# Performance work log

Measured on AMD Instinct MI355X. Metric: run time of the kernel, lower is better.

## Reference

```python
import jax, jax.numpy as jnp
import numpy as np

HARD_RATIO = 0.5
HARD_WEIGHT = 0.5
B, Q, D = 1024, 32, 512


def _l2norm(x):
    return x / jnp.linalg.norm(x, axis=-1, keepdims=True)


def setup_inputs() -> dict:
    key = jax.random.key(0)
    k1, k2 = jax.random.split(key)
    fusion_feats = _l2norm(jax.random.normal(k1, (B, D), dtype=jnp.float32))
    target_feats = _l2norm(jax.random.normal(k2, (B, Q, D), dtype=jnp.float32))
    temp = jnp.float32(0.07)
    return {"fusion_feats": fusion_feats, "target_feats": target_feats, "temp": temp}


def reference(fusion_feats, target_feats, temp):
    b = fusion_feats.shape[0]
    # sim[i, j, q] = fusion[i] . target[j, q]  -> max over query tokens q
    sim = jnp.einsum('id,jqd->ijq', fusion_feats, target_feats)  # (B, B, Q)
    sim_max = jnp.max(sim, axis=-1) / temp                        # (B, B)

    # standard InfoNCE with diagonal labels
    loss_standard = -jnp.mean(jnp.diagonal(jax.nn.log_softmax(sim_max, axis=-1)))

    # online hard-negative mining: per-row top-k over off-diagonal entries
    num_hard = max(1, int(b * HARD_RATIO))
    diag_mask = jnp.eye(b, dtype=bool)
    masked = jnp.where(diag_mask, -jnp.inf, sim_max)
    hard_sims, _ = jax.lax.top_k(masked, num_hard)                # (B, num_hard)
    pos = jnp.diagonal(sim_max)                                    # (B,)
    # -log(exp(pos) / (exp(pos) + sum exp(hard))) = logsumexp([pos, hard]) - pos
    lse = jax.nn.logsumexp(jnp.concatenate([pos[:, None], hard_sims], axis=1), axis=1)
    hard_loss_online = jnp.mean(lse - pos)

    total_loss = loss_standard + HARD_WEIGHT * hard_loss_online
    return total_loss
```

## Files before the change

### kernel.cpp

```cpp
#include <hip/hip_runtime.h>
#include <hip/hip_bf16.h>
#include <math.h>

typedef unsigned short u16;
typedef unsigned char u8;
typedef unsigned int u32;
typedef __attribute__((ext_vector_type(4))) float f32x4;
typedef __attribute__((ext_vector_type(8))) int i32x8;

__global__ void cvt_fused(const float* __restrict__ F, const float* __restrict__ T,
                          u32* __restrict__ Fb, u32* __restrict__ Tb,
                          float* __restrict__ out) {
    const int idx = blockIdx.x * blockDim.x + threadIdx.x;
    if (idx == 0) out[0] = 0.f;
    const float* s;
    u32* d;
    int i;
    if (idx < 65536) { s = F; d = Fb; i = idx; }
    else             { s = T; d = Tb; i = idx - 65536; }
    const float4 v0 = *(const float4*)(s + (size_t)i * 8);
    const float4 v1 = *(const float4*)(s + (size_t)i * 8 + 4);
    int lo = __builtin_amdgcn_cvt_pk_fp8_f32(v0.x * 16.f, v0.y * 16.f, 0, false);
    lo     = __builtin_amdgcn_cvt_pk_fp8_f32(v0.z * 16.f, v0.w * 16.f, lo, true);
    int hi = __builtin_amdgcn_cvt_pk_fp8_f32(v1.x * 16.f, v1.y * 16.f, 0, false);
    hi     = __builtin_amdgcn_cvt_pk_fp8_f32(v1.z * 16.f, v1.w * 16.f, hi, true);
    uint2 o; o.x = (u32)lo; o.y = (u32)hi;
    ((uint2*)d)[i] = o;
}

#define GLB_AS __attribute__((address_space(1)))
#define LDS_AS __attribute__((address_space(3)))

__device__ __forceinline__ void gload_lds16(const void* g, void* l) {
    __builtin_amdgcn_global_load_lds((const GLB_AS void*)g, (LDS_AS void*)l, 16, 0, 0);
}

__device__ __forceinline__ i32x8 mk8(int4 a, int4 b) {
    i32x8 r;
    r[0] = a.x; r[1] = a.y; r[2] = a.z; r[3] = a.w;
    r[4] = b.x; r[5] = b.y; r[6] = b.z; r[7] = b.w;
    return r;
}

__global__ __launch_bounds__(256, 2)
void gemm_max(const u8* __restrict__ A, const u8* __restrict__ B,
              const float* __restrict__ temp_ptr, float* __restrict__ sim) {
    __shared__ __align__(16) u8 lA[128 * 128];
    __shared__ __align__(16) u8 lB[128 * 128];
    const int bn = blockIdx.x;
    const int bm = blockIdx.y;
    const int tid  = threadIdx.x;
    const int wave = tid >> 6;
    const int lane = tid & 63;
    const int wm = wave >> 1;
    const int wn = wave & 1;

    f32x4 acc[4][4] = {};

    const int srow = lane >> 3;
    const int sch  = (lane & 7) ^ srow;
    const u8* gA0 = A + (size_t)(bm * 128 + wave * 8 + srow) * 512 + sch * 16;
    const u8* gB0 = B + (size_t)(bn * 128 + wave * 8 + srow) * 512 + sch * 16;
    u8* dA = lA + wave * 1024;
    u8* dB = lB + wave * 1024;

    const int frow = lane & 15;
    const int fq   = lane >> 4;

    for (int k0 = 0; k0 < 512; k0 += 128) {
#pragma unroll
        for (int j = 0; j < 4; ++j) {
            gload_lds16(gA0 + k0 + j * 16384, dA + j * 4096);
            gload_lds16(gB0 + k0 + j * 16384, dB + j * 4096);
        }
        __syncthreads();

        i32x8 bf[4];
#pragma unroll
        for (int t = 0; t < 4; ++t) {
            const int rb = wn * 64 + t * 16 + frow;
            const int bb = ((rb >> 3) << 10) + ((rb & 7) << 7);
            int4 p0 = *(const int4*)&lB[bb + ((((fq << 1))     ^ (rb & 7)) << 4)];
            int4 p1 = *(const int4*)&lB[bb + ((((fq << 1) | 1) ^ (rb & 7)) << 4)];
            bf[t] = mk8(p0, p1);
        }
#pragma unroll
        for (int mt = 0; mt < 4; ++mt) {
            const int ra = wm * 64 + mt * 16 + frow;
            const int ba = ((ra >> 3) << 10) + ((ra & 7) << 7);
            int4 q0 = *(const int4*)&lA[ba + ((((fq << 1))     ^ (ra & 7)) << 4)];
            int4 q1 = *(const int4*)&lA[ba + ((((fq << 1) | 1) ^ (ra & 7)) << 4)];
            const i32x8 af = mk8(q0, q1);
#pragma unroll
            for (int nt = 0; nt < 4; ++nt)
                acc[mt][nt] = __builtin_amdgcn_mfma_scale_f32_16x16x128_f8f6f4(
                    af, bf[nt], acc[mt][nt],
                    0, 0,
                    0, 0x7F,
                    0, 0x7F);
        }
        __syncthreads();
    }

    const float inv = 1.0f / (256.0f * (*temp_ptr));
    const int jb = (bn * 128 + wn * 64) >> 5;
#pragma unroll
    for (int mt = 0; mt < 4; ++mt) {
#pragma unroll
        for (int rr = 0; rr < 4; ++rr) {
            float v0 = fmaxf(acc[mt][0][rr], acc[mt][1][rr]);
            float v1 = fmaxf(acc[mt][2][rr], acc[mt][3][rr]);
#pragma unroll
            for (int off = 1; off < 16; off <<= 1) {
                v0 = fmaxf(v0, __shfl_xor(v0, off));
                v1 = fmaxf(v1, __shfl_xor(v1, off));
            }
            if ((lane & 15) == 0) {
                const int row = bm * 128 + wm * 64 + mt * 16 + fq * 4 + rr;
                sim[row * 1024 + jb]     = v0 * inv;
                sim[row * 1024 + jb + 1] = v1 * inv;
            }
        }
    }
}

__device__ __forceinline__ u32 f2key(float x) {
    u32 b = __float_as_uint(x);
    return (b & 0x80000000u) ? ~b : (b | 0x80000000u);
}
__device__ __forceinline__ float key2f(u32 k) {
    return __uint_as_float((k & 0x80000000u) ? (k & 0x7fffffffu) : ~k);
}

__global__ __launch_bounds__(256)
void row_loss(const float* __restrict__ sim, float* __restrict__ out) {
    const int tid = threadIdx.x;
    const int lane = tid & 63;
    const int wv = tid >> 6;
    const int i = blockIdx.x * 4 + wv;

    float v[16];
    const float4* rp = (const float4*)(sim + (size_t)i * 1024);
#pragma unroll
    for (int t = 0; t < 4; ++t) {
        float4 f = rp[t * 64 + lane];
        v[t * 4 + 0] = f.x; v[t * 4 + 1] = f.y; v[t * 4 + 2] = f.z; v[t * 4 + 3] = f.w;
    }

    const int dslot = ((i >> 8) << 2) | (i & 3);
    const int dlane = (i >> 2) & 63;

    u32 k[16];
#pragma unroll
    for (int t = 0; t < 16; ++t) {
        u32 kk = f2key(v[t]);
        k[t] = (lane == dlane && t == dslot) ? 0u : kk;
    }

    float pv = 0.f;
#pragma unroll
    for (int t = 0; t < 16; ++t) if (t == dslot) pv = v[t];
    const float pos = __shfl(pv, dlane);

    float m = v[0];
#pragma unroll
    for (int t = 1; t < 16; ++t) m = fmaxf(m, v[t]);
#pragma unroll
    for (int off = 32; off > 0; off >>= 1) m = fmaxf(m, __shfl_xor(m, off));
    float s = 0.f;
#pragma unroll
    for (int t = 0; t < 16; ++t) s += __expf(v[t] - m);
#pragma unroll
    for (int off = 32; off > 0; off >>= 1) s += __shfl_xor(s, off);
    const float loss_std = m + __logf(s) - pos;

    u32 lo = 0u, hi = 0xFFFFFFFFu;
    while (lo < hi) {
        const u32 span = hi - lo;
        const u32 mid = lo + (span >> 1) + (span & 1u);
        int cnt = 0;
#pragma unroll
        for (int t = 0; t < 16; ++t) cnt += (k[t] >= mid);
#pragma unroll
        for (int off = 32; off > 0; off >>= 1) cnt += __shfl_xor(cnt, off);
        if (cnt >= 512) lo = mid; else hi = mid - 1;
    }
    const u32 t_key = lo;
    const float tval = key2f(t_key);

    float se = 0.f;
    int cgt = 0;
#pragma unroll
    for (int t = 0; t < 16; ++t) {
        if (k[t] > t_key) { se += __expf(v[t] - m); ++cgt; }
    }
#pragma unroll
    for (int off = 32; off > 0; off >>= 1) se += __shfl_xor(se, off);
#pragma unroll
    for (int off = 32; off > 0; off >>= 1) cgt += __shfl_xor(cgt, off);

    const float sh = se + (float)(512 - cgt) * __expf(tval - m) + __expf(pos - m);
    const float hard = m + __logf(sh) - pos;

    if (lane == 0)
        atomicAdd(out, (loss_std + 0.5f * hard) * (1.0f / 1024.0f));
}

extern "C" void kernel_launch(void* const* d_in, const int* in_sizes, int n_in,
                              void* d_out, int out_size, void* d_ws, size_t ws_size,
                              hipStream_t stream) {
    const float* F    = (const float*)d_in[0];
    const float* T    = (const float*)d_in[1];
    const float* temp = (const float*)d_in[2];
    float* out = (float*)d_out;

    char* ws = (char*)d_ws;
    u32*  Fb8 = (u32*)ws;
    u32*  Tb8 = (u32*)(ws + (1u << 20));
    float* sim = (float*)(ws + (1u << 20) + (32u << 20));

    cvt_fused<<<8448, 256, 0, stream>>>(F, T, Fb8, Tb8, out);

    dim3 grid(256, 8);
    gemm_max<<<grid, 256, 0, stream>>>((const u8*)Fb8, (const u8*)Tb8, temp, sim);

    row_loss<<<256, 256, 0, stream>>>(sim, out);
}
```

Measured before the change: 162.0 us.

## Double-buffer LDS tiles in fp8 GEMM-max to overlap loads with MFMA

```diff
diff --git a/kernel.cpp b/kernel.cpp
--- a/kernel.cpp
+++ b/kernel.cpp
@@ -45,8 +45,8 @@
 __global__ __launch_bounds__(256, 2)
 void gemm_max(const u8* __restrict__ A, const u8* __restrict__ B,
               const float* __restrict__ temp_ptr, float* __restrict__ sim) {
-    __shared__ __align__(16) u8 lA[128 * 128];
-    __shared__ __align__(16) u8 lB[128 * 128];
+    __shared__ __align__(16) u8 lA0[16384], lB0[16384];
+    __shared__ __align__(16) u8 lA1[16384], lB1[16384];
     const int bn = blockIdx.x;
     const int bm = blockIdx.y;
     const int tid  = threadIdx.x;
@@ -58,49 +58,63 @@
     f32x4 acc[4][4] = {};
 
     const int srow = lane >> 3;
-    const int sch  = (lane & 7) ^ srow;
-    const u8* gA0 = A + (size_t)(bm * 128 + wave * 8 + srow) * 512 + sch * 16;
-    const u8* gB0 = B + (size_t)(bn * 128 + wave * 8 + srow) * 512 + sch * 16;
-    u8* dA = lA + wave * 1024;
-    u8* dB = lB + wave * 1024;
+    const int sst  = (lane & 7) ^ srow;
+    const int g    = (sst < 4) ? (2 * sst) : (2 * sst - 7);
+    const u8* gA0 = A + (size_t)(bm * 128 + wave * 8 + srow) * 512 + g * 16;
+    const u8* gB0 = B + (size_t)(bn * 128 + wave * 8 + srow) * 512 + g * 16;
+    const int lo_ = wave * 1024;
 
     const int frow = lane & 15;
     const int fq   = lane >> 4;
 
-    for (int k0 = 0; k0 < 512; k0 += 128) {
-#pragma unroll
-        for (int j = 0; j < 4; ++j) {
-            gload_lds16(gA0 + k0 + j * 16384, dA + j * 4096);
-            gload_lds16(gB0 + k0 + j * 16384, dB + j * 4096);
-        }
-        __syncthreads();
-
-        i32x8 bf[4];
-#pragma unroll
-        for (int t = 0; t < 4; ++t) {
-            const int rb = wn * 64 + t * 16 + frow;
-            const int bb = ((rb >> 3) << 10) + ((rb & 7) << 7);
-            int4 p0 = *(const int4*)&lB[bb + ((((fq << 1))     ^ (rb & 7)) << 4)];
-            int4 p1 = *(const int4*)&lB[bb + ((((fq << 1) | 1) ^ (rb & 7)) << 4)];
-            bf[t] = mk8(p0, p1);
-        }
-#pragma unroll
-        for (int mt = 0; mt < 4; ++mt) {
-            const int ra = wm * 64 + mt * 16 + frow;
-            const int ba = ((ra >> 3) << 10) + ((ra & 7) << 7);
-            int4 q0 = *(const int4*)&lA[ba + ((((fq << 1))     ^ (ra & 7)) << 4)];
-            int4 q1 = *(const int4*)&lA[ba + ((((fq << 1) | 1) ^ (ra & 7)) << 4)];
-            const i32x8 af = mk8(q0, q1);
-#pragma unroll
-            for (int nt = 0; nt < 4; ++nt)
-                acc[mt][nt] = __builtin_amdgcn_mfma_scale_f32_16x16x128_f8f6f4(
-                    af, bf[nt], acc[mt][nt],
-                    0, 0,
-                    0, 0x7F,
-                    0, 0x7F);
-        }
-        __syncthreads();
-    }
+#define STAGE(K0, DA, DB)                                                   \
+    {                                                                       \
+        _Pragma("unroll")                                                   \
+        for (int j = 0; j < 4; ++j) {                                       \
+            gload_lds16(gA0 + (K0) + j * 16384, (DA) + lo_ + j * 4096);     \
+            gload_lds16(gB0 + (K0) + j * 16384, (DB) + lo_ + j * 4096);     \
+        }                                                                   \
+    }
+
+#define COMPUTE(LA, LB)                                                     \
+    {                                                                       \
+        i32x8 bfr[4];                                                       \
+        _Pragma("unroll")                                                   \
+        for (int t = 0; t < 4; ++t) {                                       \
+            const int rb = wn * 64 + t * 16 + frow;                         \
+            const int bb = ((rb >> 3) << 10) + ((rb & 7) << 7);             \
+            int4 p0 = *(const int4*)&(LB)[bb + (((fq)     ^ (rb & 7)) << 4)]; \
+            int4 p1 = *(const int4*)&(LB)[bb + (((4 + fq) ^ (rb & 7)) << 4)]; \
+            bfr[t] = mk8(p0, p1);                                           \
+        }                                                                   \
+        _Pragma("unroll")                                                   \
+        for (int mt = 0; mt < 4; ++mt) {                                    \
+            const int ra = wm * 64 + mt * 16 + frow;                        \
+            const int ba = ((ra >> 3) << 10) + ((ra & 7) << 7);             \
+            int4 q0 = *(const int4*)&(LA)[ba + (((fq)     ^ (ra & 7)) << 4)]; \
+            int4 q1 = *(const int4*)&(LA)[ba + (((4 + fq) ^ (ra & 7)) << 4)]; \
+            const i32x8 afr = mk8(q0, q1);                                  \
+            _Pragma("unroll")                                               \
+            for (int nt = 0; nt < 4; ++nt)                                  \
+                acc[mt][nt] = __builtin_amdgcn_mfma_scale_f32_16x16x128_f8f6f4( \
+                    afr, bfr[nt], acc[mt][nt], 0, 0, 0, 0x7F, 0, 0x7F);     \
+        }                                                                   \
+    }
+
+    STAGE(0, lA0, lB0);
+    __syncthreads();
+    STAGE(128, lA1, lB1);
+    COMPUTE(lA0, lB0);
+    __syncthreads();
+    STAGE(256, lA0, lB0);
+    COMPUTE(lA1, lB1);
+    __syncthreads();
+    STAGE(384, lA1, lB1);
+    COMPUTE(lA0, lB0);
+    __syncthreads();
+    COMPUTE(lA1, lB1);
+#undef STAGE
+#undef COMPUTE
 
     const float inv = 1.0f / (256.0f * (*temp_ptr));
     const int jb = (bn * 128 + wn * 64) >> 5;
@@ -117,8 +131,8 @@
             }
             if ((lane & 15) == 0) {
                 const int row = bm * 128 + wm * 64 + mt * 16 + fq * 4 + rr;
-                sim[row * 1024 + jb]     = v0 * inv;
-                sim[row * 1024 + jb + 1] = v1 * inv;
+                __builtin_nontemporal_store(v0 * inv, &sim[row * 1024 + jb]);
+                __builtin_nontemporal_store(v1 * inv, &sim[row * 1024 + jb + 1]);
             }
         }
     }
```

Result: no change. 159.7 us (-1.4%).
